# Kernel optimization log

Hardware: AMD Instinct MI355X
Metric: run time of the kernel (lower is better)

Reference implementation:

```python
import jax, jax.numpy as jnp
import numpy as np

# BatchNorm1d in eval mode with default init (gamma=1, beta=0, mean=0, var=1):
# y = x / sqrt(1 + eps)
BN_S = 1.0 / float(np.sqrt(1.0 + 1e-5))
ROI_THRESH = 0.8
DN = ('NCHW', 'OIHW', 'NCHW')


def conv(x, w, stride=1, pad=1):
    return jax.lax.conv_general_dilated(x, w, (stride, stride), ((pad, pad), (pad, pad)), dimension_numbers=DN)


def inv_conv(x, w):
    # dense equivalent of spconv.SparseInverseConv2d paired with a stride-2, pad-1, k=3 conv:
    # adjoint index map = transposed conv (lhs_dilation=2, flipped kernel, pad (1,2))
    return jax.lax.conv_general_dilated(x, jnp.flip(w, (2, 3)), (1, 1), ((1, 2), (1, 2)), lhs_dilation=(2, 2), dimension_numbers=DN)


def downsample_mask(m):
    # active-site generation rule of a stride-2, pad-1, k=3 sparse conv == 3x3/stride-2 max pool
    return jax.lax.reduce_window(m, 0.0, jax.lax.max, (1, 1, 3, 3), (1, 1, 2, 2), ((0, 0), (0, 0), (1, 1), (1, 1)))


def setup_inputs():
    key = jax.random.key(0)
    ks = jax.random.split(key, 24)
    b, n_i, H, W = 2, 4, 384, 384
    s = 0.1  # weight scale to keep activations bounded through the conv stack
    inp = {
        'x': jax.random.normal(ks[0], (b, 64, H // 4, W // 4), jnp.float32),
        'image': jax.random.normal(ks[1], (b, 3, H, W), jnp.float32),
        'masks': jax.random.uniform(ks[2], (b, n_i, H, W), jnp.float32),
        'roi_masks': jax.random.uniform(ks[3], (b, n_i, H, W), jnp.float32),
        'w1a': jax.random.normal(ks[4], (32, 4, 3, 3), jnp.float32) * s,
        'w1b': jax.random.normal(ks[5], (32, 32, 3, 3), jnp.float32) * s,
        'w2a': jax.random.normal(ks[6], (32, 32, 3, 3), jnp.float32) * s,
        'w2b': jax.random.normal(ks[7], (32, 32, 3, 3), jnp.float32) * s,
        'w4a': jax.random.normal(ks[8], (64, 32, 3, 3), jnp.float32) * s,
        'w4b': jax.random.normal(ks[9], (64, 64, 3, 3), jnp.float32) * s,
        'inv4_w': jax.random.normal(ks[10], (64, 64, 3, 3), jnp.float32) * s,
        'l4_sub_w': jax.random.normal(ks[11], (32, 64, 3, 3), jnp.float32) * s,
        'inv2_w': jax.random.normal(ks[12], (32, 32, 3, 3), jnp.float32) * s,
        'l5_sub_w': jax.random.normal(ks[13], (32, 32, 3, 3), jnp.float32) * s,
        'r4_w1': jax.random.normal(ks[14], (32, 64, 3, 3), jnp.float32) * s,
        'r4_w2': jax.random.normal(ks[15], (1, 32, 3, 3), jnp.float32) * s,
        'r4_b2': jax.random.normal(ks[16], (1,), jnp.float32) * s,
        'r1_w1': jax.random.normal(ks[17], (32, 32, 3, 3), jnp.float32) * s,
        'r1_w2': jax.random.normal(ks[18], (1, 32, 3, 3), jnp.float32) * s,
        'r1_b2': jax.random.normal(ks[19], (1,), jnp.float32) * s,
    }
    return inp


def reference(x, image, masks, roi_masks, w1a, w1b, w2a, w2b, w4a, w4b, inv4_w, l4_sub_w, inv2_w, l5_sub_w, r4_w1, r4_w2, r4_b2, r1_w1, r1_w2, r1_b2):
    # Faithful dense emulation of predict_details: SubMConv == conv(masked x)*mask,
    # stride-2 SparseConv == conv(masked x) masked by max-pooled mask,
    # SparseInverseConv == transposed conv masked by parent-resolution mask,
    # Fsp.sparse_add on shared indices == masked add, dense()-99/+99 == where(mask, v, -99).
    b, n_i, H, W = masks.shape
    N = b * n_i
    m = masks.reshape(N, 1, H, W)
    roi = roi_masks.reshape(N, 1, H, W)
    img = jnp.broadcast_to(image[:, None], (b, n_i, 3, H, W)).reshape(N, 3, H, W)
    inp = jnp.concatenate([img, m], axis=1)  # [N,4,H,W]

    mask1 = (roi > ROI_THRESH).astype(inp.dtype)
    mask2 = downsample_mask(mask1)
    mask4 = downsample_mask(mask2)

    # low_os1_module: SubMConv, ReLU, BN, SubMConv, ReLU, BN
    f = jnp.maximum(conv(inp * mask1, w1a) * mask1, 0.0) * BN_S
    fea1 = jnp.maximum(conv(f, w1b) * mask1, 0.0) * BN_S  # [N,32,H,W]
    # low_os2_module: stride-2 SparseConv, ReLU, BN, SubMConv, ReLU, BN
    g = jnp.maximum(conv(fea1, w2a, stride=2) * mask2, 0.0) * BN_S
    fea2 = jnp.maximum(conv(g, w2b) * mask2, 0.0) * BN_S  # [N,32,H/2,W/2]
    # low_os4_module
    h = jnp.maximum(conv(fea2, w4a, stride=2) * mask4, 0.0) * BN_S
    fea3 = jnp.maximum(conv(h, w4b) * mask4, 0.0) * BN_S  # [N,64,H/4,W/4]

    # gather dense OS4 features at sparse sites (batch index // n_i) + sparse_add
    xg = jnp.broadcast_to(x[:, None], (b, n_i) + x.shape[1:]).reshape(N, *x.shape[1:]) * mask4
    xs = xg + fea3

    # refine_OS4: SubMConv, BN, leaky, SubMConv(+bias); dense() with -99 off-support
    t = jax.nn.leaky_relu(conv(xs, r4_w1) * mask4 * BN_S, 0.2)
    t = (conv(t, r4_w2) + r4_b2[None, :, None, None]) * mask4
    x_os4_out = jnp.where(mask4 > 0, t, -99.0)

    # layer4: SparseInverseConv(64->64) to OS2 sites, BN, leaky, SubMConv(64->32); add fea2
    u = jax.nn.leaky_relu(inv_conv(xs, inv4_w) * mask2 * BN_S, 0.2)
    u = conv(u, l4_sub_w) * mask2 + fea2
    # layer5: SparseInverseConv(32->32) to OS1 sites, BN, leaky, SubMConv(32->32); add fea1
    v = jax.nn.leaky_relu(inv_conv(u, inv2_w) * mask1 * BN_S, 0.2)
    v = conv(v, l5_sub_w) * mask1 + fea1

    # refine_OS1
    t1 = jax.nn.leaky_relu(conv(v, r1_w1) * mask1 * BN_S, 0.2)
    t1 = (conv(t1, r1_w2) + r1_b2[None, :, None, None]) * mask1
    x_os1_out = jnp.where(mask1 > 0, t1, -99.0)
    return x_os4_out, x_os1_out
```

## Files before the change

kernel.cpp:

```cpp
#include <hip/hip_runtime.h>
#include <hip/hip_bf16.h>

using bf16 = __hip_bfloat16;
typedef unsigned char u8;
typedef short bf16x8 __attribute__((ext_vector_type(8)));
typedef short bf16x4 __attribute__((ext_vector_type(4)));
typedef float f32x4 __attribute__((ext_vector_type(4)));

#define BNS 0.9999950000374997f
#define MFMA_B16 __builtin_amdgcn_mfma_f32_16x16x32_bf16

__device__ __forceinline__ short f2bs(float v){ bf16 h = __float2bfloat16(v); return *reinterpret_cast<short*>(&h); }
__device__ __forceinline__ float s2f(short s){ union{unsigned u; float f;} x; x.u = ((unsigned)(unsigned short)s) << 16; return x.f; }
__device__ __forceinline__ float lrelu(float a){ return fmaxf(a, 0.2f*a); }
__device__ __forceinline__ bf16x8 ld8(const short* p){ return *(const bf16x8*)(p); }


__global__ __launch_bounds__(256) void k_mask1(const float* __restrict__ roi, u8* __restrict__ m1, int total){
    int i = blockIdx.x*256 + threadIdx.x;
    if (i < total) m1[i] = (roi[i] > 0.8f) ? 1 : 0;
}

__global__ __launch_bounds__(256) void k_down(const u8* __restrict__ mi, u8* __restrict__ mo,
                                              int IH, int IW, int OH, int OW){
    int p = blockIdx.x*256 + threadIdx.x;
    int n = blockIdx.y;
    if (p >= OH*OW) return;
    int oy = p / OW, ox = p - oy*OW;
    const u8* src = mi + (size_t)n*IH*IW;
    int v = 0;
    #pragma unroll
    for (int ky=0; ky<3; ky++){
        int iy = 2*oy + ky - 1;
        if ((unsigned)iy >= (unsigned)IH) continue;
        #pragma unroll
        for (int kx=0; kx<3; kx++){
            int ix = 2*ox + kx - 1;
            if ((unsigned)ix < (unsigned)IW) v |= src[iy*IW + ix];
        }
    }
    mo[(size_t)n*OH*OW + p] = (u8)v;
}

__global__ __launch_bounds__(256) void k_wprep(const float* __restrict__ w1b,
                                               const float* __restrict__ i2,
                                               const float* __restrict__ l5,
                                               const float* __restrict__ r1a,
                                               const float* __restrict__ w2b,
                                               const float* __restrict__ w2a,
                                               short* __restrict__ dst){
    int a = blockIdx.y;
    const float* src = (a==0)? w1b : (a==1)? i2 : (a==2)? l5 : (a==3)? r1a : (a==4)? w2b : w2a;
    float sc = (a==2) ? 1.0f : BNS;
    int j = blockIdx.x*256 + threadIdx.x;
    if (j < 9216){
        int co = j/288, r = j%288, ci = r/9, k = r%9;
        dst[a*9216 + k*1024 + co*32 + ci] = f2bs(src[j]*sc);
    }
}

__global__ __launch_bounds__(256) void k_wprep4(const float* __restrict__ inv4,
                                                const float* __restrict__ w4b,
                                                const float* __restrict__ l4s,
                                                const float* __restrict__ r4w1,
                                                const float* __restrict__ w4a,
                                                short* __restrict__ dst)
{
    int a = blockIdx.y;
    int j = blockIdx.x*256 + threadIdx.x;
    if (a < 2){
        if (j < 36864){
            int co = j/576, r = j%576, ci = r/9, k = r%9;
            const float* s = a ? w4b : inv4;
            dst[a*36864 + k*4096 + co*64 + ci] = f2bs(s[j]*BNS);
        }
    } else if (a < 4){
        if (j < 18432){
            int co = j/576, r = j%576, ci = r/9, k = r%9;
            const float* s = (a==2) ? l4s : r4w1;
            float sc = (a==2) ? 1.0f : BNS;
            dst[73728 + (a-2)*18432 + k*2048 + co*64 + ci] = f2bs(s[j]*sc);
        }
    } else {
        if (j < 18432){
            int co = j/288, r = j%288, ci = r/9, k = r%9;
            dst[110592 + k*2048 + co*32 + ci] = f2bs(w4a[j]*BNS);
        }
    }
}

__global__ __launch_bounds__(256) void k_wprep_misc(const float* __restrict__ w1a,
                                                    const float* __restrict__ r1w2,
                                                    const float* __restrict__ r4w2,
                                                    short* __restrict__ d1a,
                                                    short* __restrict__ dh){
    int a = blockIdx.y;
    int j = blockIdx.x*256 + threadIdx.x;
    if (a == 0){
        if (j < 2048){
            int h = j >> 10, r = j & 1023, co = r >> 5, kq = r & 31;
            int q = h*32 + kq;
            d1a[j] = (q < 36) ? f2bs(w1a[co*36 + q]*BNS) : 0;
        }
    } else {
        if (j < 4608){
            int k = j/512, r = j%512, co = r/32, ci = r%32;
            const float* s = (a==1) ? r1w2 : r4w2;
            dh[(a-1)*4608 + j] = (co == 0) ? f2bs(s[ci*9 + k]) : 0;
        }
    }
}

template<int CIN, int COUT, int EPI, int TH>
__global__ __launch_bounds__(256) void mconv_s1(const short* __restrict__ in, int H,
                                                const short* __restrict__ wT,
                                                const u8* __restrict__ mask,
                                                const float* __restrict__ res32,
                                                short* __restrict__ out, int tilesX)
{
    const int HW = H*H;
    const int HV = CIN/32, G = COUT/16, CH8 = CIN/8;
    const int SR = TH + 2;
    const int SITES = SR*18;
    const int PS = (SITES | 1)*8;
    const int U2N = TH/4;
    int tY = blockIdx.x / tilesX, tX = blockIdx.x % tilesX, n = blockIdx.z;
    int y0 = tY*TH, x0 = tX*16;

    __shared__ __align__(16) short s_in[CH8*((SITES|1)*8)];
    __shared__ u8 s_m[TH*16];

    int tid = threadIdx.x;
    const short* inN = in + (size_t)n*HW*CIN;
    for (int i = tid; i < SITES*CH8; i += 256){
        int r = i/CH8, q = i%CH8;
        int ry = r/18, rx = r%18;
        int gy = y0-1+ry, gx = x0-1+rx;
        bf16x8 v = {0,0,0,0,0,0,0,0};
        if ((unsigned)gy < (unsigned)H && (unsigned)gx < (unsigned)H)
            v = *(const bf16x8*)(inN + ((size_t)gy*H + gx)*CIN + q*8);
        *(bf16x8*)(s_in + q*PS + r*8) = v;
    }
    for (int i = tid; i < TH*16; i += 256){
        int ty = i>>4, tx = i&15;
        s_m[i] = mask[(size_t)n*HW + (y0+ty)*H + x0+tx];
    }
    __syncthreads();

    int wv = tid >> 6, lane = tid & 63;
    int nQ = lane >> 4, nn = lane & 15;

    f32x4 acc[U2N][G];
    #pragma unroll
    for (int u2=0; u2<U2N; ++u2)
        #pragma unroll
        for (int g=0; g<G; ++g) acc[u2][g] = (f32x4){0,0,0,0};

    #pragma unroll
    for (int h=0; h<HV; ++h){
        const short* bh[U2N];
        #pragma unroll
        for (int u2=0; u2<U2N; ++u2){
            int ty = u2*4 + wv;
            bh[u2] = s_in + (h*4+nQ)*PS + (ty*18 + nn)*8;
        }
        #pragma unroll
        for (int ky=0; ky<3; ++ky)
            #pragma unroll
            for (int kx=0; kx<3; ++kx){
                const int k = ky*3+kx;
                bf16x8 a[G];
                #pragma unroll
                for (int g=0; g<G; ++g)
                    a[g] = *(const bf16x8*)(wT + k*COUT*CIN + (g*16+nn)*CIN + h*32 + nQ*8);
                #pragma unroll
                for (int u2=0; u2<U2N; ++u2){
                    bf16x8 bfr = ld8(bh[u2] + (ky*18+kx)*8);
                    #pragma unroll
                    for (int g=0; g<G; ++g)
                        acc[u2][g] = MFMA_B16(a[g], bfr, acc[u2][g], 0,0,0);
                }
            }
    }

    #pragma unroll
    for (int u2=0; u2<U2N; ++u2){
        int nt = u2*4 + wv;
        int p = (y0+nt)*H + x0+nn;
        u8 m = s_m[nt*16 + nn];
        short* op = out + ((size_t)n*HW + p)*COUT;
        #pragma unroll
        for (int g=0; g<G; ++g){
            float r[4];
            #pragma unroll
            for (int e=0; e<4; ++e){
                int co = g*16 + nQ*4 + e;
                float a = acc[u2][g][e], o;
                if      (EPI == 0) o = m ? fmaxf(a,0.f) : 0.f;
                else if (EPI == 1) o = m ? lrelu(a) : 0.f;
                else o = m ? fmaxf(a,0.f) + res32[((size_t)(n>>2)*COUT + co)*(size_t)HW + p] : 0.f;
                r[e] = o;
            }
            bf16x4 w4 = {f2bs(r[0]),f2bs(r[1]),f2bs(r[2]),f2bs(r[3])};
            *(bf16x4*)(op + g*16 + nQ*4) = w4;
        }
    }
}

template<int TH>
__global__ __launch_bounds__(256) void mconv_head32(const short* __restrict__ in, int H,
                                                    const short* __restrict__ wTh,
                                                    const float* __restrict__ bias,
                                                    const u8* __restrict__ mask,
                                                    float* __restrict__ out, int tilesX)
{
    const int HW = H*H;
    const int SR = TH + 2, SITES = SR*18;
    const int PS = (SITES|1)*8;
    int tY = blockIdx.x / tilesX, tX = blockIdx.x % tilesX, n = blockIdx.z;
    int y0 = tY*TH, x0 = tX*16;

    __shared__ __align__(16) short s_in[4*((SITES|1)*8)];
    __shared__ u8 s_m[TH*16];

    int tid = threadIdx.x;
    const short* inN = in + (size_t)n*HW*32;
    for (int i = tid; i < SITES*4; i += 256){
        int r = i>>2, q = i&3;
        int ry = r/18, rx = r%18;
        int gy = y0-1+ry, gx = x0-1+rx;
        bf16x8 v = {0,0,0,0,0,0,0,0};
        if ((unsigned)gy < (unsigned)H && (unsigned)gx < (unsigned)H)
            v = *(const bf16x8*)(inN + ((size_t)gy*H + gx)*32 + q*8);
        *(bf16x8*)(s_in + q*PS + r*8) = v;
    }
    for (int i = tid; i < TH*16; i += 256){
        int ty = i>>4, tx = i&15;
        s_m[i] = mask[(size_t)n*HW + (y0+ty)*H + x0+tx];
    }
    __syncthreads();

    int wv = tid >> 6, lane = tid & 63;
    int nQ = lane >> 4, nn = lane & 15;
    float bb = bias[0];

    for (int nt = wv; nt < TH; nt += 4){
        const short* bp = s_in + nQ*PS + (nt*18 + nn)*8;
        f32x4 acc = {0,0,0,0};
        #pragma unroll
        for (int ky=0; ky<3; ++ky)
            #pragma unroll
            for (int kx=0; kx<3; ++kx){
                const int k = ky*3+kx;
                bf16x8 aw = *(const bf16x8*)(wTh + k*512 + nn*32 + nQ*8);
                bf16x8 bfr = ld8(bp + (ky*18+kx)*8);
                acc = MFMA_B16(aw, bfr, acc, 0,0,0);
            }
        if (nQ == 0){
            u8 m = s_m[nt*16 + nn];
            int p = (y0+nt)*H + x0+nn;
            out[(size_t)n*HW + p] = m ? acc[0] + bb : -99.f;
        }
    }
}

template<int COUT, int THO>
__global__ __launch_bounds__(256) void mconv_s2m(const short* __restrict__ in, int IH,
                                                 const short* __restrict__ wT,
                                                 const u8* __restrict__ mask,
                                                 short* __restrict__ out, int OH, int tilesX)
{
    const int IHW = IH*IH, OHW = OH*OH, G = COUT/16;
    const int IR = 2*THO + 1;
    const int SITES = IR*33;
    const int PS = (SITES|1)*8;
    const int ITN = THO/4;
    int tY = blockIdx.x / tilesX, tX = blockIdx.x % tilesX, n = blockIdx.z;
    int y0 = tY*THO, x0 = tX*16;

    __shared__ __align__(16) short s_in[4*((SITES|1)*8)];
    __shared__ u8 s_m[THO*16];

    int tid = threadIdx.x;
    const short* inN = in + (size_t)n*IHW*32;
    for (int i = tid; i < SITES*4; i += 256){
        int r = i>>2, q = i&3;
        int ry = r/33, rx = r%33;
        int gy = 2*y0-1+ry, gx = 2*x0-1+rx;
        bf16x8 v = {0,0,0,0,0,0,0,0};
        if ((unsigned)gy < (unsigned)IH && (unsigned)gx < (unsigned)IH)
            v = *(const bf16x8*)(inN + ((size_t)gy*IH + gx)*32 + q*8);
        *(bf16x8*)(s_in + q*PS + r*8) = v;
    }
    for (int i = tid; i < THO*16; i += 256){
        int ty = i>>4, tx = i&15;
        s_m[i] = mask[(size_t)n*OHW + (y0+ty)*OH + x0+tx];
    }
    __syncthreads();

    int wv = tid >> 6, lane = tid & 63;
    int nQ = lane >> 4, nn = lane & 15;

    f32x4 acc[ITN][G];
    #pragma unroll
    for (int it=0; it<ITN; ++it)
        #pragma unroll
        for (int g=0; g<G; ++g) acc[it][g] = (f32x4){0,0,0,0};

    const short* pb[ITN];
    #pragma unroll
    for (int it=0; it<ITN; ++it){
        int nt = it*4 + wv;
        pb[it] = s_in + nQ*PS + ((2*nt)*33 + 2*nn)*8;
    }

    #pragma unroll
    for (int ky=0; ky<3; ++ky)
        #pragma unroll
        for (int kx=0; kx<3; ++kx){
            const int k = ky*3+kx;
            bf16x8 a[G];
            #pragma unroll
            for (int g=0; g<G; ++g)
                a[g] = *(const bf16x8*)(wT + k*COUT*32 + (g*16+nn)*32 + nQ*8);
            #pragma unroll
            for (int it=0; it<ITN; ++it){
                bf16x8 bfr = ld8(pb[it] + (ky*33+kx)*8);
                #pragma unroll
                for (int g=0; g<G; ++g)
                    acc[it][g] = MFMA_B16(a[g], bfr, acc[it][g], 0,0,0);
            }
        }

    #pragma unroll
    for (int it=0; it<ITN; ++it){
        int nt = it*4 + wv;
        int p = (y0+nt)*OH + x0+nn;
        u8 m = s_m[nt*16 + nn];
        short* op = out + ((size_t)n*OHW + p)*COUT;
        #pragma unroll
        for (int g=0; g<G; ++g){
            float r[4];
            #pragma unroll
            for (int e=0; e<4; ++e) r[e] = m ? fmaxf(acc[it][g][e],0.f) : 0.f;
            bf16x4 w4 = {f2bs(r[0]),f2bs(r[1]),f2bs(r[2]),f2bs(r[3])};
            *(bf16x4*)(op + g*16 + nQ*4) = w4;
        }
    }
}

__global__ __launch_bounds__(256) void conv1ab3(const float* __restrict__ image,
                                                const float* __restrict__ masks,
                                                const u8*  __restrict__ M1,
                                                const short* __restrict__ wT1a,
                                                const short* __restrict__ wT1b,
                                                short* __restrict__ fea1)
{
    const int H = 384; const int HW = H*H;
    const int PS = 181*8;
    int tY = blockIdx.x / 48, tX = blockIdx.x % 48, n = blockIdx.z;
    int y0 = tY*16, x0 = tX*8;

    __shared__ float s_inp[4][240];
    __shared__ u8    s_m[240];
    __shared__ __align__(16) short s_ic[8*(181*8)];
    short* s_f = s_ic;

    int tid = threadIdx.x;
    for (int i = tid; i < 240; i += 256){
        int ly = i/12, lxx = i%12;
        int gy = y0-2+ly, gx = x0-2+lxx;
        bool inb = ((unsigned)gy < 384u) && ((unsigned)gx < 384u);
        u8 mv = inb ? M1[(size_t)n*HW + gy*H + gx] : 0;
        s_m[i] = mv;
        float mm = (float)mv;
        int p = gy*H + gx;
        #pragma unroll
        for (int c = 0; c < 4; ++c){
            float v = 0.f;
            if (inb) v = (c < 3) ? image[((size_t)(n>>2)*3 + c)*HW + p]
                                 : masks[(size_t)n*HW + p];
            s_inp[c][i] = v*mm;
        }
    }
    __syncthreads();

    for (int i = tid; i < 180*64; i += 256){
        int site = i >> 6, q = i & 63;
        short v = 0;
        if (q < 36){
            int ci = q/9, k = q - ci*9, ky = k/3, kx = k - ky*3;
            int fy = site/10, fx = site - fy*10;
            v = f2bs(s_inp[ci][(fy+ky)*12 + fx+kx]);
        }
        s_ic[(q>>3)*PS + site*8 + (q&7)] = v;
    }
    __syncthreads();

    int wv = tid >> 6, lane = tid & 63;
    int nQ = lane >> 4, nn = lane & 15;

    f32x4 fr[3][2];
    {
        #pragma unroll
        for (int u=0; u<3; ++u){ fr[u][0] = (f32x4){0,0,0,0}; fr[u][1] = (f32x4){0,0,0,0}; }
        #pragma unroll
        for (int h=0; h<2; ++h){
            bf16x8 fa0 = *(const bf16x8*)(wT1a + h*1024 + nn*32 + nQ*8);
            bf16x8 fa1 = *(const bf16x8*)(wT1a + h*1024 + (16+nn)*32 + nQ*8);
            #pragma unroll
            for (int u=0; u<3; ++u){
                int nt = u*4 + wv;
                int s0 = nt*16 + nn;
                int s = s0 > 179 ? 179 : s0;
                bf16x8 bfr = ld8(s_ic + (h*4+nQ)*PS + s*8);
                fr[u][0] = MFMA_B16(fa0, bfr, fr[u][0], 0,0,0);
                fr[u][1] = MFMA_B16(fa1, bfr, fr[u][1], 0,0,0);
            }
        }
    }
    __syncthreads();

    #pragma unroll
    for (int u=0; u<3; ++u){
        int nt = u*4 + wv;
        int s0 = nt*16 + nn;
        if (s0 <= 179){
            int fy = s0/10, fx = s0 - fy*10;
            u8 m = s_m[(fy+1)*12 + fx+1];
            #pragma unroll
            for (int g=0; g<2; ++g){
                float r[4];
                #pragma unroll
                for (int e=0; e<4; ++e){
                    float a = fr[u][g][e];
                    r[e] = m ? fmaxf(a,0.f) : 0.f;
                }
                bf16x4 w4 = {f2bs(r[0]),f2bs(r[1]),f2bs(r[2]),f2bs(r[3])};
                *(bf16x4*)(s_f + (g*2 + (nQ>>1))*PS + s0*8 + (nQ&1)*4) = w4;
            }
        }
    }
    __syncthreads();

    {
        f32x4 acc0[2], acc1[2];
        const short* pb[2];
        #pragma unroll
        for (int it=0; it<2; ++it){
            acc0[it] = (f32x4){0,0,0,0}; acc1[it] = (f32x4){0,0,0,0};
            int s0 = (it*4 + wv)*16 + nn;
            int ty = s0 >> 3, tx = s0 & 7;
            pb[it] = s_f + nQ*PS + (ty*10 + tx)*8;
        }
        #pragma unroll
        for (int ky=0; ky<3; ++ky)
            #pragma unroll
            for (int kx=0; kx<3; ++kx){
                const int k = ky*3+kx;
                bf16x8 a0 = *(const bf16x8*)(wT1b + k*1024 + nn*32 + nQ*8);
                bf16x8 a1 = *(const bf16x8*)(wT1b + k*1024 + (16+nn)*32 + nQ*8);
                #pragma unroll
                for (int it=0; it<2; ++it){
                    bf16x8 bfr = ld8(pb[it] + (ky*10+kx)*8);
                    acc0[it] = MFMA_B16(a0, bfr, acc0[it], 0,0,0);
                    acc1[it] = MFMA_B16(a1, bfr, acc1[it], 0,0,0);
                }
            }
        #pragma unroll
        for (int it=0; it<2; ++it){
            int s0 = (it*4 + wv)*16 + nn;
            int ty = s0 >> 3, tx = s0 & 7;
            u8 m = s_m[(ty+2)*12 + tx+2];
            short* fp = fea1 + ((size_t)n*HW + (size_t)(y0+ty)*H + (x0+tx))*32;
            #pragma unroll
            for (int g=0; g<2; ++g){
                float r[4];
                #pragma unroll
                for (int e=0; e<4; ++e){
                    float a = g ? acc1[it][e] : acc0[it][e];
                    r[e] = m ? fmaxf(a,0.f) : 0.f;
                }
                bf16x4 w4 = {f2bs(r[0]),f2bs(r[1]),f2bs(r[2]),f2bs(r[3])};
                *(bf16x4*)(fp + g*16 + nQ*4) = w4;
            }
        }
    }
}

__global__ __launch_bounds__(256) void fk_l4c(const short* __restrict__ xs,
                                              const short* __restrict__ fea2,
                                              const u8*  __restrict__ M2,
                                              const short* __restrict__ wTi4,
                                              const short* __restrict__ wTl4,
                                              short* __restrict__ u_out)
{
    const int H2 = 192, HW2 = H2*H2, H4 = 96, HW4 = H4*H4;
    const int PSX = 101*8, PSU = 325*8;
    int tY = blockIdx.x / 12, tX = blockIdx.x % 12, n = blockIdx.z;
    int y0 = tY*16, x0 = tX*16;
    int uy0 = (y0>>1) - 1, ux0 = (x0>>1) - 1;

    __shared__ __align__(16) short s_xs[8*(101*8)];
    __shared__ __align__(16) short s_ul[8*(325*8)];
    __shared__ u8 s_m[324];

    int tid = threadIdx.x;
    const short* xN = xs + (size_t)n*HW4*64;
    for (int i = tid; i < 100*8; i += 256){
        int r = i>>3, q = i&7;
        int ly = r/10, lxx = r%10;
        int gy = uy0+ly, gx = ux0+lxx;
        bf16x8 v = {0,0,0,0,0,0,0,0};
        if ((unsigned)gy < 96u && (unsigned)gx < 96u)
            v = *(const bf16x8*)(xN + ((size_t)gy*H4 + gx)*64 + q*8);
        *(bf16x8*)(s_xs + q*PSX + r*8) = v;
    }
    for (int i = tid; i < 324; i += 256){
        int ry = i/18, rx = i%18; int gy = y0-1+ry, gx = x0-1+rx;
        s_m[i] = ((unsigned)gy < 192u && (unsigned)gx < 192u) ? M2[(size_t)n*HW2 + gy*H2 + gx] : 0;
    }

    int wv = tid >> 6, lane = tid & 63;
    int nQ = lane >> 4, nn = lane & 15;

    bf16x4 pf2v[4][2];
    {
        const short* f2N = fea2 + (size_t)n*HW2*32;
        #pragma unroll
        for (int u2=0; u2<4; ++u2){
            int nt = u2*4 + wv;
            int p = (y0+nt)*H2 + x0+nn;
            const short* fp = f2N + (size_t)p*32;
            pf2v[u2][0] = *(const bf16x4*)(fp + nQ*4);
            pf2v[u2][1] = *(const bf16x4*)(fp + 16 + nQ*4);
        }
    }
    __syncthreads();

    for (int ui = wv; ui < 24; ui += 4){
        int cls = ui/6, nt = ui%6;
        int pY = cls >> 1, pX = cls & 1;
        int s0 = nt*16 + nn;
        int s = s0 > 80 ? 80 : s0;
        int jr = s/9, jc = s%9;
        int ry = 2*jr + pY, rx = 2*jc + pX;

        int tiy[4], tix[4], twk[4]; int tapN;
        if (pY == 0){
            if (pX == 0){
                tiy[0]=jr;   tix[0]=jc;   twk[0]=8;
                tiy[1]=jr;   tix[1]=jc+1; twk[1]=6;
                tiy[2]=jr+1; tix[2]=jc;   twk[2]=2;
                tiy[3]=jr+1; tix[3]=jc+1; twk[3]=0; tapN=4;
            } else {
                tiy[0]=jr;   tix[0]=jc+1; twk[0]=7;
                tiy[1]=jr+1; tix[1]=jc+1; twk[1]=1; tapN=2;
            }
        } else {
            if (pX == 0){
                tiy[0]=jr+1; tix[0]=jc;   twk[0]=5;
                tiy[1]=jr+1; tix[1]=jc+1; twk[1]=3; tapN=2;
            } else {
                tiy[0]=jr+1; tix[0]=jc+1; twk[0]=4; tapN=1;
            }
        }

        f32x4 acc[4];
        #pragma unroll
        for (int g=0; g<4; ++g) acc[g] = (f32x4){0,0,0,0};
        for (int t = 0; t < tapN; ++t){
            int off = (tiy[t]*10 + tix[t])*8;
            bf16x8 xlo = ld8(s_xs + nQ*PSX + off);
            bf16x8 xhi = ld8(s_xs + (4+nQ)*PSX + off);
            const short* wk = wTi4 + twk[t]*4096;
            #pragma unroll
            for (int g=0; g<4; ++g){
                bf16x8 alo = *(const bf16x8*)(wk + (g*16+nn)*64 + nQ*8);
                bf16x8 ahi = *(const bf16x8*)(wk + (g*16+nn)*64 + 32 + nQ*8);
                acc[g] = MFMA_B16(alo, xlo, acc[g], 0,0,0);
                acc[g] = MFMA_B16(ahi, xhi, acc[g], 0,0,0);
            }
        }
        if (s0 <= 80){
            int sidx = ry*18 + rx;
            u8 m = s_m[sidx];
            #pragma unroll
            for (int g=0; g<4; ++g){
                float r[4];
                #pragma unroll
                for (int e=0; e<4; ++e){
                    float a = acc[g][e];
                    r[e] = m ? lrelu(a) : 0.f;
                }
                bf16x4 w4 = {f2bs(r[0]),f2bs(r[1]),f2bs(r[2]),f2bs(r[3])};
                *(bf16x4*)(s_ul + ((g>>1)*4 + (g&1)*2 + (nQ>>1))*PSU + sidx*8 + (nQ&1)*4) = w4;
            }
        }
    }
    __syncthreads();

    {
        f32x4 acc0[4], acc1[4];
        const short* pv[4];
        #pragma unroll
        for (int u2=0; u2<4; ++u2){
            acc0[u2] = (f32x4){0,0,0,0}; acc1[u2] = (f32x4){0,0,0,0};
            int nt = u2*4 + wv;
            pv[u2] = s_ul + nQ*PSU + (nt*18 + nn)*8;
        }
        #pragma unroll
        for (int ky=0; ky<3; ++ky)
            #pragma unroll
            for (int kx=0; kx<3; ++kx){
                int k = ky*3+kx;
                const short* wk = wTl4 + k*2048;
                bf16x8 a0lo = *(const bf16x8*)(wk + nn*64 + nQ*8);
                bf16x8 a0hi = *(const bf16x8*)(wk + nn*64 + 32 + nQ*8);
                bf16x8 a1lo = *(const bf16x8*)(wk + (16+nn)*64 + nQ*8);
                bf16x8 a1hi = *(const bf16x8*)(wk + (16+nn)*64 + 32 + nQ*8);
                #pragma unroll
                for (int u2=0; u2<4; ++u2){
                    bf16x8 vlo = ld8(pv[u2] + (ky*18+kx)*8);
                    bf16x8 vhi = ld8(pv[u2] + 4*PSU + (ky*18+kx)*8);
                    acc0[u2] = MFMA_B16(a0lo, vlo, acc0[u2], 0,0,0);
                    acc0[u2] = MFMA_B16(a0hi, vhi, acc0[u2], 0,0,0);
                    acc1[u2] = MFMA_B16(a1lo, vlo, acc1[u2], 0,0,0);
                    acc1[u2] = MFMA_B16(a1hi, vhi, acc1[u2], 0,0,0);
                }
            }
        #pragma unroll
        for (int u2 = 0; u2 < 4; ++u2){
            int nt = u2*4 + wv;
            int p = (y0+nt)*H2 + x0+nn;
            u8 m = s_m[(nt+1)*18 + nn+1];
            short* up = u_out + ((size_t)n*HW2 + p)*32;
            #pragma unroll
            for (int g=0; g<2; ++g){
                float r[4];
                #pragma unroll
                for (int e=0; e<4; ++e){
                    float a = g ? acc1[u2][e] : acc0[u2][e];
                    r[e] = m ? a + s2f(pf2v[u2][g][e]) : 0.f;
                }
                bf16x4 w4 = {f2bs(r[0]),f2bs(r[1]),f2bs(r[2]),f2bs(r[3])};
                *(bf16x4*)(up + g*16 + nQ*4) = w4;
            }
        }
    }
}

__global__ __launch_bounds__(256) void fk_back8(const short* __restrict__ u,
                                                const short* __restrict__ fea1,
                                                const u8*  __restrict__ M1,
                                                const short* __restrict__ wTi2,
                                                const short* __restrict__ wTl5,
                                                const short* __restrict__ wTr1a,
                                                const short* __restrict__ wTr1b,
                                                const float* __restrict__ r1_b2,
                                                float* __restrict__ out1)
{
    const int H1 = 384, HW1 = H1*H1, H2 = 192, HW2 = H2*H2;
    const int PS_U = 97*8, PS_A = 309*8, PS_B = 241*8, PS_C = 181*8;
    int tY = blockIdx.x / 48, tX = blockIdx.x % 48, n = blockIdx.z;
    int y0 = tY*16, x0 = tX*8;
    int uy0 = (y0>>1) - 2, ux0 = (x0>>1) - 2;

    __shared__ __align__(16) short sP0[4*(309*8)];
    __shared__ __align__(16) short sP1[4*(241*8)];
    __shared__ u8 s_m[308];
    short* s_u  = sP1;
    short* s_vl = sP0;
    short* s_v  = sP1;
    short* s_t1 = sP0;

    int tid = threadIdx.x;
    const short* uN = u + (size_t)n*HW2*32;
    for (int i = tid; i < 96*4; i += 256){
        int r = i>>2, q = i&3;
        int ly = r >> 3, lxx = r & 7;
        int gy = uy0+ly, gx = ux0+lxx;
        bf16x8 v = {0,0,0,0,0,0,0,0};
        if ((unsigned)gy < 192u && (unsigned)gx < 192u)
            v = *(const bf16x8*)(uN + ((size_t)gy*H2 + gx)*32 + q*8);
        *(bf16x8*)(s_u + q*PS_U + r*8) = v;
    }
    for (int i = tid; i < 308; i += 256){
        int ry = i/14, rx = i%14; int gy = y0-3+ry, gx = x0-3+rx;
        s_m[i] = ((unsigned)gy < 384u && (unsigned)gx < 384u) ? M1[(size_t)n*HW1 + gy*H1 + gx] : 0;
    }

    int wv = tid >> 6, lane = tid & 63;
    int nQ = lane >> 4, nn = lane & 15;

    bf16x4 pf[4][2];
    {
        #pragma unroll
        for (int u2=0; u2<4; ++u2){
            int nt = u2*4 + wv;
            if (nt < 15){
                int s0 = nt*16 + nn;
                int vy = s0/12, vx = s0%12;
                int gY = y0-2+vy, gX = x0-2+vx;
                int gyc = gY < 0 ? 0 : (gY > 383 ? 383 : gY);
                int gxc = gX < 0 ? 0 : (gX > 383 ? 383 : gX);
                const short* f1 = fea1 + ((size_t)n*HW1 + (size_t)gyc*H1 + gxc)*32;
                pf[u2][0] = *(const bf16x4*)(f1 + nQ*4);
                pf[u2][1] = *(const bf16x4*)(f1 + 16 + nQ*4);
            }
        }
    }
    __syncthreads();

    for (int ui = wv; ui < 20; ui += 4){
        int cls = ui/5, nt = ui%5;
        int pY = cls >> 1, pX = cls & 1;
        int s0 = nt*16 + nn;
        int s = s0 > 76 ? 76 : s0;
        int jr = s/7, jc = s%7;
        int ry = 2*jr + pY, rx = 2*jc + pX;

        int tiy[4], tix[4], twk[4]; int tapN;
        if (pY == 0){
            if (pX == 0){
                tiy[0]=jr;   tix[0]=jc;   twk[0]=8;
                tiy[1]=jr;   tix[1]=jc+1; twk[1]=6;
                tiy[2]=jr+1; tix[2]=jc;   twk[2]=2;
                tiy[3]=jr+1; tix[3]=jc+1; twk[3]=0; tapN=4;
            } else {
                tiy[0]=jr;   tix[0]=jc+1; twk[0]=7;
                tiy[1]=jr+1; tix[1]=jc+1; twk[1]=1; tapN=2;
            }
        } else {
            if (pX == 0){
                tiy[0]=jr+1; tix[0]=jc;   twk[0]=5;
                tiy[1]=jr+1; tix[1]=jc+1; twk[1]=3; tapN=2;
            } else {
                tiy[0]=jr+1; tix[0]=jc+1; twk[0]=4; tapN=1;
            }
        }

        f32x4 acc0 = {0,0,0,0}, acc1 = {0,0,0,0};
        for (int t = 0; t < tapN; ++t){
            bf16x8 bfr = ld8(s_u + nQ*PS_U + (tiy[t]*8 + tix[t])*8);
            bf16x8 a0 = *(const bf16x8*)(wTi2 + twk[t]*1024 + nn*32 + nQ*8);
            bf16x8 a1 = *(const bf16x8*)(wTi2 + twk[t]*1024 + (16+nn)*32 + nQ*8);
            acc0 = MFMA_B16(a0, bfr, acc0, 0,0,0);
            acc1 = MFMA_B16(a1, bfr, acc1, 0,0,0);
        }
        if (s0 <= 76){
            int sidx = ry*14 + rx;
            u8 m = s_m[sidx];
            float r[8];
            #pragma unroll
            for (int g=0; g<2; ++g)
                #pragma unroll
                for (int e=0; e<4; ++e){
                    float a = g ? acc1[e] : acc0[e];
                    r[g*4+e] = m ? lrelu(a) : 0.f;
                }
            bf16x4 w0 = {f2bs(r[0]),f2bs(r[1]),f2bs(r[2]),f2bs(r[3])};
            bf16x4 w1 = {f2bs(r[4]),f2bs(r[5]),f2bs(r[6]),f2bs(r[7])};
            *(bf16x4*)(s_vl + (nQ>>1)*PS_A     + sidx*8 + (nQ&1)*4) = w0;
            *(bf16x4*)(s_vl + (2+(nQ>>1))*PS_A + sidx*8 + (nQ&1)*4) = w1;
        }
    }
    __syncthreads();

    {
        f32x4 acc0[4], acc1[4];
        const short* pv[4]; bool act[4];
        #pragma unroll
        for (int u2=0; u2<4; ++u2){
            acc0[u2] = (f32x4){0,0,0,0}; acc1[u2] = (f32x4){0,0,0,0};
            int nt = u2*4 + wv;
            act[u2] = (nt < 15);
            int s0 = act[u2] ? nt*16 + nn : 0;
            int vy = s0/12, vx = s0%12;
            pv[u2] = s_vl + nQ*PS_A + (vy*14 + vx)*8;
        }
        #pragma unroll
        for (int ky=0; ky<3; ++ky)
            #pragma unroll
            for (int kx=0; kx<3; ++kx){
                const int k = ky*3+kx;
                bf16x8 wb0 = *(const bf16x8*)(wTl5 + k*1024 + nn*32 + nQ*8);
                bf16x8 wb1 = *(const bf16x8*)(wTl5 + k*1024 + (16+nn)*32 + nQ*8);
                #pragma unroll
                for (int u2=0; u2<4; ++u2){
                    bf16x8 bfr = ld8(pv[u2] + (ky*14+kx)*8);
                    acc0[u2] = MFMA_B16(wb0, bfr, acc0[u2], 0,0,0);
                    acc1[u2] = MFMA_B16(wb1, bfr, acc1[u2], 0,0,0);
                }
            }
        #pragma unroll
        for (int u2 = 0; u2 < 4; ++u2){
            if (!act[u2]) continue;
            int s0 = (u2*4 + wv)*16 + nn;
            int vy = s0/12, vx = s0%12;
            u8 m = s_m[(vy+1)*14 + vx+1];
            float r[8];
            #pragma unroll
            for (int g=0; g<2; ++g)
                #pragma unroll
                for (int e=0; e<4; ++e){
                    float a = g ? acc1[u2][e] : acc0[u2][e];
                    r[g*4+e] = m ? a + s2f(pf[u2][g][e]) : 0.f;
                }
            bf16x4 w0 = {f2bs(r[0]),f2bs(r[1]),f2bs(r[2]),f2bs(r[3])};
            bf16x4 w1 = {f2bs(r[4]),f2bs(r[5]),f2bs(r[6]),f2bs(r[7])};
            *(bf16x4*)(s_v + (nQ>>1)*PS_B     + s0*8 + (nQ&1)*4) = w0;
            *(bf16x4*)(s_v + (2+(nQ>>1))*PS_B + s0*8 + (nQ&1)*4) = w1;
        }
    }
    __syncthreads();

    {
        f32x4 acc0[3], acc1[3];
        const short* pt[3];
        #pragma unroll
        for (int t=0; t<3; ++t){
            acc0[t] = (f32x4){0,0,0,0}; acc1[t] = (f32x4){0,0,0,0};
            int s0 = (wv + t*4)*16 + nn;
            int s = s0 > 179 ? 179 : s0;
            int qy = s/10, qx = s%10;
            pt[t] = s_v + nQ*PS_B + (qy*12 + qx)*8;
        }
        #pragma unroll
        for (int ky=0; ky<3; ++ky)
            #pragma unroll
            for (int kx=0; kx<3; ++kx){
                const int k = ky*3+kx;
                bf16x8 wc0 = *(const bf16x8*)(wTr1a + k*1024 + nn*32 + nQ*8);
                bf16x8 wc1 = *(const bf16x8*)(wTr1a + k*1024 + (16+nn)*32 + nQ*8);
                #pragma unroll
                for (int t=0; t<3; ++t){
                    bf16x8 bfr = ld8(pt[t] + (ky*12+kx)*8);
                    acc0[t] = MFMA_B16(wc0, bfr, acc0[t], 0,0,0);
                    acc1[t] = MFMA_B16(wc1, bfr, acc1[t], 0,0,0);
                }
            }
        #pragma unroll
        for (int t=0; t<3; ++t){
            int s0 = (wv + t*4)*16 + nn;
            if (s0 <= 179){
                int qy = s0/10, qx = s0%10;
                u8 m = s_m[(qy+2)*14 + qx+2];
                float r[8];
                #pragma unroll
                for (int g=0; g<2; ++g)
                    #pragma unroll
                    for (int e=0; e<4; ++e){
                        float a = g ? acc1[t][e] : acc0[t][e];
                        r[g*4+e] = m ? lrelu(a) : 0.f;
                    }
                bf16x4 w0 = {f2bs(r[0]),f2bs(r[1]),f2bs(r[2]),f2bs(r[3])};
                bf16x4 w1 = {f2bs(r[4]),f2bs(r[5]),f2bs(r[6]),f2bs(r[7])};
                *(bf16x4*)(s_t1 + (nQ>>1)*PS_C     + s0*8 + (nQ&1)*4) = w0;
                *(bf16x4*)(s_t1 + (2+(nQ>>1))*PS_C + s0*8 + (nQ&1)*4) = w1;
            }
        }
    }
    __syncthreads();

    {
        float bb = r1_b2[0];
        f32x4 acc[2];
        const short* pt1[2];
        #pragma unroll
        for (int u2=0; u2<2; ++u2){
            acc[u2] = (f32x4){0,0,0,0};
            int s0 = (u2*4 + wv)*16 + nn;
            int ty = s0 >> 3, tx = s0 & 7;
            pt1[u2] = s_t1 + nQ*PS_C + (ty*10 + tx)*8;
        }
        #pragma unroll
        for (int ky=0; ky<3; ++ky)
            #pragma unroll
            for (int kx=0; kx<3; ++kx){
                const int k = ky*3+kx;
                bf16x8 aw = *(const bf16x8*)(wTr1b + k*512 + nn*32 + nQ*8);
                #pragma unroll
                for (int u2=0; u2<2; ++u2){
                    bf16x8 bfr = ld8(pt1[u2] + (ky*10+kx)*8);
                    acc[u2] = MFMA_B16(aw, bfr, acc[u2], 0,0,0);
                }
            }
        if (nQ == 0){
            #pragma unroll
            for (int u2=0; u2<2; ++u2){
                int s0 = (u2*4 + wv)*16 + nn;
                int ty = s0 >> 3, tx = s0 & 7;
                u8 m = s_m[(ty+3)*14 + tx+3];
                float o = m ? acc[u2][0] + bb : -99.f;
                out1[(size_t)n*HW1 + (y0+ty)*H1 + (x0+tx)] = o;
            }
        }
    }
}


extern "C" void kernel_launch(void* const* d_in, const int* in_sizes, int n_in,
                              void* d_out, int out_size, void* d_ws, size_t ws_size,
                              hipStream_t stream)
{
    const float* x      = (const float*)d_in[0];
    const float* image  = (const float*)d_in[1];
    const float* masks  = (const float*)d_in[2];
    const float* roi    = (const float*)d_in[3];
    const float* w1a    = (const float*)d_in[4];
    const float* w1b    = (const float*)d_in[5];
    const float* w2a    = (const float*)d_in[6];
    const float* w2b    = (const float*)d_in[7];
    const float* w4a    = (const float*)d_in[8];
    const float* w4b    = (const float*)d_in[9];
    const float* inv4_w = (const float*)d_in[10];
    const float* l4_sub = (const float*)d_in[11];
    const float* inv2_w = (const float*)d_in[12];
    const float* l5_sub = (const float*)d_in[13];
    const float* r4_w1  = (const float*)d_in[14];
    const float* r4_w2  = (const float*)d_in[15];
    const float* r4_b2  = (const float*)d_in[16];
    const float* r1_w1  = (const float*)d_in[17];
    const float* r1_w2  = (const float*)d_in[18];
    const float* r1_b2  = (const float*)d_in[19];
    float* out = (float*)d_out;

    const int N = 8;
    const int H1 = 384, HW1 = 384*384;
    const int H2 = 192, HW2 = 192*192;
    const int H4 = 96,  HW4 = 96*96;

    char* wsp = (char*)d_ws;
    size_t off = 0;
    auto alloc = [&](size_t bytes) -> char* {
        char* p = wsp + off;
        off += (bytes + 255) & ~(size_t)255;
        return p;
    };
    bf16* FEA1 = (bf16*)alloc((size_t)N*32*HW1*2);
    u8*   M1   = (u8*)alloc((size_t)N*HW1);
    u8*   M2   = (u8*)alloc((size_t)N*HW2);
    u8*   M4   = (u8*)alloc((size_t)N*HW4);
    bf16* FEA2 = (bf16*)alloc((size_t)N*32*HW2*2);
    bf16* XS   = (bf16*)alloc((size_t)N*64*HW4*2);
    bf16* GU   = (bf16*)alloc((size_t)N*32*HW2*2);
    bf16* HT   = (bf16*)alloc((size_t)N*64*HW4*2);
    short* WT   = (short*)alloc(6*9216*2);
    short* WT4  = (short*)alloc((size_t)129024*2);
    short* WT1a = (short*)alloc(2048*2);
    short* WTh  = (short*)alloc(2*4608*2);
    (void)ws_size; (void)in_sizes; (void)n_in; (void)out_size;

    short* wT1b  = WT;
    short* wTi2  = WT + 9216;
    short* wTl5  = WT + 2*9216;
    short* wTr1a = WT + 3*9216;
    short* wT2b  = WT + 4*9216;
    short* wT2a  = WT + 5*9216;
    short* wTi4  = WT4;
    short* wT4b  = WT4 + 36864;
    short* wTl4  = WT4 + 73728;
    short* wTr4a = WT4 + 92160;
    short* wT4a  = WT4 + 110592;
    short* wTr1b = WTh;
    short* wTr4b = WTh + 4608;

    dim3 blk(256);

    k_mask1<<<dim3((N*HW1 + 255)/256), blk, 0, stream>>>(roi, M1, N*HW1);
    k_down<<<dim3((HW2 + 255)/256, N), blk, 0, stream>>>(M1, M2, H1, H1, H2, H2);
    k_down<<<dim3((HW4 + 255)/256, N), blk, 0, stream>>>(M2, M4, H2, H2, H4, H4);
    k_wprep<<<dim3(36, 6), blk, 0, stream>>>(w1b, inv2_w, l5_sub, r1_w1, w2b, w2a, WT);
    k_wprep4<<<dim3(144, 5), blk, 0, stream>>>(inv4_w, w4b, l4_sub, r4_w1, w4a, WT4);
    k_wprep_misc<<<dim3(18, 3), blk, 0, stream>>>(w1a, r1_w2, r4_w2, WT1a, WTh);

    conv1ab3<<<dim3(1152, 1, N), blk, 0, stream>>>(image, masks, M1, WT1a, wT1b, (short*)FEA1);
    mconv_s2m<32,8><<<dim3(288, 1, N), blk, 0, stream>>>((const short*)FEA1, H1, wT2a, M2, (short*)GU, H2, 12);
    mconv_s1<32,32,0,8><<<dim3(288, 1, N), blk, 0, stream>>>((const short*)GU, H2, wT2b, M2, nullptr, (short*)FEA2, 12);
    mconv_s2m<64,4><<<dim3(144, 1, N), blk, 0, stream>>>((const short*)FEA2, H2, wT4a, M4, (short*)HT, H4, 6);
    mconv_s1<64,64,3,4><<<dim3(144, 1, N), blk, 0, stream>>>((const short*)HT, H4, wT4b, M4, x, (short*)XS, 6);

    mconv_s1<64,32,1,4><<<dim3(144, 1, N), blk, 0, stream>>>((const short*)XS, H4, wTr4a, M4, nullptr, (short*)HT, 6);
    mconv_head32<4><<<dim3(144, 1, N), blk, 0, stream>>>((const short*)HT, H4, wTr4b, r4_b2, M4, out, 6);

    fk_l4c<<<dim3(144, 1, N), blk, 0, stream>>>((const short*)XS, (const short*)FEA2, M2,
                                                wTi4, wTl4, (short*)GU);

    fk_back8<<<dim3(1152, 1, N), blk, 0, stream>>>((const short*)GU, (const short*)FEA1, M1,
                                                   wTi2, wTl5, wTr1a, wTr1b, r1_b2,
                                                   out + (size_t)N*HW4);
}
```

Before: 606.3 us.

## Compact active sites per stage in fused OS1 kernel to skip masked MFMA work

The fused OS1 kernel now builds per-stage lists of active (mask=1) sites in shared memory with atomic counters, and runs each MFMA conv stage only over compacted 16-site groups of active positions instead of every position in the tile. Inactive output pixels are written as -99 up front, and the staging buffers are zero-filled before each stage so inactive neighbours read as zero. With about 20% active sites this is meant to cut matrix work substantially. In exchange it adds list-building passes, atomics, extra zero-fill loops and barriers, a per-wave imbalance in the inverse-conv stage (one parity class per wave), and fea1 loads that are now issued inside the loop rather than prefetched.

Result: faster. 551.3 us (-9.1%).

```diff
diff --git a/kernel.cpp b/kernel.cpp
--- a/kernel.cpp
+++ b/kernel.cpp
@@ -669,18 +669,26 @@
     __shared__ __align__(16) short sP0[4*(309*8)];
     __shared__ __align__(16) short sP1[4*(241*8)];
     __shared__ u8 s_m[308];
+    __shared__ int s_cnt[7];
+    __shared__ unsigned s_lA[4*80];
+    __shared__ unsigned s_lB[240];
+    __shared__ unsigned s_lC[180];
+    __shared__ unsigned s_lD[128];
     short* s_u  = sP1;
     short* s_vl = sP0;
     short* s_v  = sP1;
     short* s_t1 = sP0;
 
     int tid = threadIdx.x;
+    const bf16x8 Z8 = {0,0,0,0,0,0,0,0};
+
+    if (tid < 7) s_cnt[tid] = 0;
     const short* uN = u + (size_t)n*HW2*32;
     for (int i = tid; i < 96*4; i += 256){
         int r = i>>2, q = i&3;
         int ly = r >> 3, lxx = r & 7;
         int gy = uy0+ly, gx = ux0+lxx;
-        bf16x8 v = {0,0,0,0,0,0,0,0};
+        bf16x8 v = Z8;
         if ((unsigned)gy < 192u && (unsigned)gx < 192u)
             v = *(const bf16x8*)(uN + ((size_t)gy*H2 + gx)*32 + q*8);
         *(bf16x8*)(s_u + q*PS_U + r*8) = v;
@@ -689,175 +697,165 @@
         int ry = i/14, rx = i%14; int gy = y0-3+ry, gx = x0-3+rx;
         s_m[i] = ((unsigned)gy < 384u && (unsigned)gx < 384u) ? M1[(size_t)n*HW1 + gy*H1 + gx] : 0;
     }
+    for (int i = tid; i < 4*309; i += 256)
+        *(bf16x8*)(s_vl + i*8) = Z8;
+    __syncthreads();
+
+    for (int i = tid; i < 308; i += 256){
+        if (s_m[i]){
+            int ry = i/14, rx = i - ry*14;
+            int cls = ((ry&1)<<1) | (rx&1);
+            int jr = ry>>1, jc = rx>>1;
+            int idx = atomicAdd(&s_cnt[cls], 1);
+            s_lA[cls*80 + idx] = ((unsigned)i<<16) | (unsigned)(jr*8+jc);
+        }
+    }
+    for (int i = tid; i < 240; i += 256){
+        int vy = i/12, vx = i - vy*12;
+        if (s_m[(vy+1)*14 + vx+1]){
+            int idx = atomicAdd(&s_cnt[4], 1);
+            s_lB[idx] = ((unsigned)i<<16) | (unsigned)(vy*14+vx);
+        }
+    }
+    for (int i = tid; i < 180; i += 256){
+        int qy = i/10, qx = i - qy*10;
+        if (s_m[(qy+2)*14 + qx+2]){
+            int idx = atomicAdd(&s_cnt[5], 1);
+            s_lC[idx] = ((unsigned)i<<16) | (unsigned)(qy*12+qx);
+        }
+    }
+    for (int i = tid; i < 128; i += 256){
+        int ty = i>>3, tx = i&7;
+        if (s_m[(ty+3)*14 + tx+3]){
+            int idx = atomicAdd(&s_cnt[6], 1);
+            s_lD[idx] = ((unsigned)i<<16) | (unsigned)(ty*10+tx);
+        } else {
+            out1[(size_t)n*HW1 + (size_t)(y0+ty)*H1 + (x0+tx)] = -99.f;
+        }
+    }
+    __syncthreads();
 
     int wv = tid >> 6, lane = tid & 63;
     int nQ = lane >> 4, nn = lane & 15;
 
-    bf16x4 pf[4][2];
     {
-        #pragma unroll
-        for (int u2=0; u2<4; ++u2){
-            int nt = u2*4 + wv;
-            if (nt < 15){
-                int s0 = nt*16 + nn;
-                int vy = s0/12, vx = s0%12;
-                int gY = y0-2+vy, gX = x0-2+vx;
-                int gyc = gY < 0 ? 0 : (gY > 383 ? 383 : gY);
-                int gxc = gX < 0 ? 0 : (gX > 383 ? 383 : gX);
-                const short* f1 = fea1 + ((size_t)n*HW1 + (size_t)gyc*H1 + gxc)*32;
-                pf[u2][0] = *(const bf16x4*)(f1 + nQ*4);
-                pf[u2][1] = *(const bf16x4*)(f1 + 16 + nQ*4);
-            }
-        }
-    }
-    __syncthreads();
-
-    for (int ui = wv; ui < 20; ui += 4){
-        int cls = ui/5, nt = ui%5;
-        int pY = cls >> 1, pX = cls & 1;
-        int s0 = nt*16 + nn;
-        int s = s0 > 76 ? 76 : s0;
-        int jr = s/7, jc = s%7;
-        int ry = 2*jr + pY, rx = 2*jc + pX;
-
-        int tiy[4], tix[4], twk[4]; int tapN;
-        if (pY == 0){
-            if (pX == 0){
-                tiy[0]=jr;   tix[0]=jc;   twk[0]=8;
-                tiy[1]=jr;   tix[1]=jc+1; twk[1]=6;
-                tiy[2]=jr+1; tix[2]=jc;   twk[2]=2;
-                tiy[3]=jr+1; tix[3]=jc+1; twk[3]=0; tapN=4;
-            } else {
-                tiy[0]=jr;   tix[0]=jc+1; twk[0]=7;
-                tiy[1]=jr+1; tix[1]=jc+1; twk[1]=1; tapN=2;
-            }
-        } else {
-            if (pX == 0){
-                tiy[0]=jr+1; tix[0]=jc;   twk[0]=5;
-                tiy[1]=jr+1; tix[1]=jc+1; twk[1]=3; tapN=2;
-            } else {
-                tiy[0]=jr+1; tix[0]=jc+1; twk[0]=4; tapN=1;
-            }
-        }
-
-        f32x4 acc0 = {0,0,0,0}, acc1 = {0,0,0,0};
-        for (int t = 0; t < tapN; ++t){
-            bf16x8 bfr = ld8(s_u + nQ*PS_U + (tiy[t]*8 + tix[t])*8);
-            bf16x8 a0 = *(const bf16x8*)(wTi2 + twk[t]*1024 + nn*32 + nQ*8);
-            bf16x8 a1 = *(const bf16x8*)(wTi2 + twk[t]*1024 + (16+nn)*32 + nQ*8);
-            acc0 = MFMA_B16(a0, bfr, acc0, 0,0,0);
-            acc1 = MFMA_B16(a1, bfr, acc1, 0,0,0);
-        }
-        if (s0 <= 76){
-            int sidx = ry*14 + rx;
-            u8 m = s_m[sidx];
-            float r[8];
-            #pragma unroll
-            for (int g=0; g<2; ++g)
-                #pragma unroll
-                for (int e=0; e<4; ++e){
-                    float a = g ? acc1[e] : acc0[e];
-                    r[g*4+e] = m ? lrelu(a) : 0.f;
-                }
-            bf16x4 w0 = {f2bs(r[0]),f2bs(r[1]),f2bs(r[2]),f2bs(r[3])};
-            bf16x4 w1 = {f2bs(r[4]),f2bs(r[5]),f2bs(r[6]),f2bs(r[7])};
-            *(bf16x4*)(s_vl + (nQ>>1)*PS_A     + sidx*8 + (nQ&1)*4) = w0;
-            *(bf16x4*)(s_vl + (2+(nQ>>1))*PS_A + sidx*8 + (nQ&1)*4) = w1;
-        }
-    }
-    __syncthreads();
-
-    {
-        f32x4 acc0[4], acc1[4];
-        const short* pv[4]; bool act[4];
-        #pragma unroll
-        for (int u2=0; u2<4; ++u2){
-            acc0[u2] = (f32x4){0,0,0,0}; acc1[u2] = (f32x4){0,0,0,0};
-            int nt = u2*4 + wv;
-            act[u2] = (nt < 15);
-            int s0 = act[u2] ? nt*16 + nn : 0;
-            int vy = s0/12, vx = s0%12;
-            pv[u2] = s_vl + nQ*PS_A + (vy*14 + vx)*8;
-        }
-        #pragma unroll
-        for (int ky=0; ky<3; ++ky)
-            #pragma unroll
-            for (int kx=0; kx<3; ++kx){
-                const int k = ky*3+kx;
-                bf16x8 wb0 = *(const bf16x8*)(wTl5 + k*1024 + nn*32 + nQ*8);
-                bf16x8 wb1 = *(const bf16x8*)(wTl5 + k*1024 + (16+nn)*32 + nQ*8);
-                #pragma unroll
-                for (int u2=0; u2<4; ++u2){
-                    bf16x8 bfr = ld8(pv[u2] + (ky*14+kx)*8);
-                    acc0[u2] = MFMA_B16(wb0, bfr, acc0[u2], 0,0,0);
-                    acc1[u2] = MFMA_B16(wb1, bfr, acc1[u2], 0,0,0);
-                }
-            }
-        #pragma unroll
-        for (int u2 = 0; u2 < 4; ++u2){
-            if (!act[u2]) continue;
-            int s0 = (u2*4 + wv)*16 + nn;
-            int vy = s0/12, vx = s0%12;
-            u8 m = s_m[(vy+1)*14 + vx+1];
-            float r[8];
-            #pragma unroll
-            for (int g=0; g<2; ++g)
-                #pragma unroll
-                for (int e=0; e<4; ++e){
-                    float a = g ? acc1[u2][e] : acc0[u2][e];
-                    r[g*4+e] = m ? a + s2f(pf[u2][g][e]) : 0.f;
-                }
-            bf16x4 w0 = {f2bs(r[0]),f2bs(r[1]),f2bs(r[2]),f2bs(r[3])};
-            bf16x4 w1 = {f2bs(r[4]),f2bs(r[5]),f2bs(r[6]),f2bs(r[7])};
-            *(bf16x4*)(s_v + (nQ>>1)*PS_B     + s0*8 + (nQ&1)*4) = w0;
-            *(bf16x4*)(s_v + (2+(nQ>>1))*PS_B + s0*8 + (nQ&1)*4) = w1;
-        }
-    }
-    __syncthreads();
-
-    {
-        f32x4 acc0[3], acc1[3];
-        const short* pt[3];
-        #pragma unroll
-        for (int t=0; t<3; ++t){
-            acc0[t] = (f32x4){0,0,0,0}; acc1[t] = (f32x4){0,0,0,0};
-            int s0 = (wv + t*4)*16 + nn;
-            int s = s0 > 179 ? 179 : s0;
-            int qy = s/10, qx = s%10;
-            pt[t] = s_v + nQ*PS_B + (qy*12 + qx)*8;
-        }
-        #pragma unroll
-        for (int ky=0; ky<3; ++ky)
-            #pragma unroll
-            for (int kx=0; kx<3; ++kx){
-                const int k = ky*3+kx;
-                bf16x8 wc0 = *(const bf16x8*)(wTr1a + k*1024 + nn*32 + nQ*8);
-                bf16x8 wc1 = *(const bf16x8*)(wTr1a + k*1024 + (16+nn)*32 + nQ*8);
-                #pragma unroll
-                for (int t=0; t<3; ++t){
-                    bf16x8 bfr = ld8(pt[t] + (ky*12+kx)*8);
-                    acc0[t] = MFMA_B16(wc0, bfr, acc0[t], 0,0,0);
-                    acc1[t] = MFMA_B16(wc1, bfr, acc1[t], 0,0,0);
-                }
-            }
-        #pragma unroll
-        for (int t=0; t<3; ++t){
-            int s0 = (wv + t*4)*16 + nn;
-            if (s0 <= 179){
-                int qy = s0/10, qx = s0%10;
-                u8 m = s_m[(qy+2)*14 + qx+2];
+        const int tN_[4]   = {4,2,2,1};
+        const int tOff[4][4] = {{0,1,8,9},{1,9,9,9},{8,9,9,9},{9,9,9,9}};
+        const int tWk [4][4] = {{8,6,2,0},{7,1,1,1},{5,3,3,3},{4,4,4,4}};
+        int cnt = s_cnt[wv];
+        int tn = tN_[wv];
+        for (int base = 0; base < cnt; base += 16){
+            int slot = base + nn;
+            bool on = slot < cnt;
+            unsigned e = s_lA[wv*80 + (on ? slot : 0)];
+            int rb = e & 0xffff;
+            f32x4 acc0 = {0,0,0,0}, acc1 = {0,0,0,0};
+            for (int t = 0; t < tn; ++t){
+                bf16x8 bfr = ld8(s_u + nQ*PS_U + (rb + tOff[wv][t])*8);
+                const short* wp = wTi2 + tWk[wv][t]*1024;
+                bf16x8 a0 = *(const bf16x8*)(wp + nn*32 + nQ*8);
+                bf16x8 a1 = *(const bf16x8*)(wp + (16+nn)*32 + nQ*8);
+                acc0 = MFMA_B16(a0, bfr, acc0, 0,0,0);
+                acc1 = MFMA_B16(a1, bfr, acc1, 0,0,0);
+            }
+            if (on){
+                int sidx = e >> 16;
                 float r[8];
                 #pragma unroll
                 for (int g=0; g<2; ++g)
                     #pragma unroll
-                    for (int e=0; e<4; ++e){
-                        float a = g ? acc1[t][e] : acc0[t][e];
-                        r[g*4+e] = m ? lrelu(a) : 0.f;
-                    }
+                    for (int ee=0; ee<4; ++ee)
+                        r[g*4+ee] = lrelu(g ? acc1[ee] : acc0[ee]);
                 bf16x4 w0 = {f2bs(r[0]),f2bs(r[1]),f2bs(r[2]),f2bs(r[3])};
                 bf16x4 w1 = {f2bs(r[4]),f2bs(r[5]),f2bs(r[6]),f2bs(r[7])};
-                *(bf16x4*)(s_t1 + (nQ>>1)*PS_C     + s0*8 + (nQ&1)*4) = w0;
-                *(bf16x4*)(s_t1 + (2+(nQ>>1))*PS_C + s0*8 + (nQ&1)*4) = w1;
+                *(bf16x4*)(s_vl + (nQ>>1)*PS_A     + sidx*8 + (nQ&1)*4) = w0;
+                *(bf16x4*)(s_vl + (2+(nQ>>1))*PS_A + sidx*8 + (nQ&1)*4) = w1;
+            }
+        }
+    }
+    __syncthreads();
+
+    for (int i = tid; i < 4*241; i += 256)
+        *(bf16x8*)(s_v + i*8) = Z8;
+    __syncthreads();
+
+    {
+        int cnt = s_cnt[4];
+        for (int base = wv*16; base < cnt; base += 64){
+            int slot = base + nn;
+            bool on = slot < cnt;
+            unsigned e = s_lB[on ? slot : 0];
+            int rb = e & 0xffff;
+            int wr = e >> 16;
+            int vy = wr/12, vx = wr - vy*12;
+            const short* f1 = fea1 + ((size_t)n*HW1 + (size_t)(y0-2+vy)*H1 + (x0-2+vx))*32;
+            bf16x4 p0 = *(const bf16x4*)(f1 + nQ*4);
+            bf16x4 p1 = *(const bf16x4*)(f1 + 16 + nQ*4);
+            const short* pv = s_vl + nQ*PS_A + rb*8;
+            f32x4 acc0 = {0,0,0,0}, acc1 = {0,0,0,0};
+            #pragma unroll
+            for (int ky=0; ky<3; ++ky)
+                #pragma unroll
+                for (int kx=0; kx<3; ++kx){
+                    const int k = ky*3+kx;
+                    bf16x8 wb0 = *(const bf16x8*)(wTl5 + k*1024 + nn*32 + nQ*8);
+                    bf16x8 wb1 = *(const bf16x8*)(wTl5 + k*1024 + (16+nn)*32 + nQ*8);
+                    bf16x8 bfr = ld8(pv + (ky*14+kx)*8);
+                    acc0 = MFMA_B16(wb0, bfr, acc0, 0,0,0);
+                    acc1 = MFMA_B16(wb1, bfr, acc1, 0,0,0);
+                }
+            if (on){
+                float r[8];
+                #pragma unroll
+                for (int ee=0; ee<4; ++ee){
+                    r[ee]   = acc0[ee] + s2f(p0[ee]);
+                    r[4+ee] = acc1[ee] + s2f(p1[ee]);
+                }
+                bf16x4 w0 = {f2bs(r[0]),f2bs(r[1]),f2bs(r[2]),f2bs(r[3])};
+                bf16x4 w1 = {f2bs(r[4]),f2bs(r[5]),f2bs(r[6]),f2bs(r[7])};
+                *(bf16x4*)(s_v + (nQ>>1)*PS_B     + wr*8 + (nQ&1)*4) = w0;
+                *(bf16x4*)(s_v + (2+(nQ>>1))*PS_B + wr*8 + (nQ&1)*4) = w1;
+            }
+        }
+    }
+    __syncthreads();
+
+    for (int i = tid; i < 4*181; i += 256)
+        *(bf16x8*)(s_t1 + i*8) = Z8;
+    __syncthreads();
+
+    {
+        int cnt = s_cnt[5];
+        for (int base = wv*16; base < cnt; base += 64){
+            int slot = base + nn;
+            bool on = slot < cnt;
+            unsigned e = s_lC[on ? slot : 0];
+            int rb = e & 0xffff;
+            const short* pv = s_v + nQ*PS_B + rb*8;
+            f32x4 acc0 = {0,0,0,0}, acc1 = {0,0,0,0};
+            #pragma unroll
+            for (int ky=0; ky<3; ++ky)
+                #pragma unroll
+                for (int kx=0; kx<3; ++kx){
+                    const int k = ky*3+kx;
+                    bf16x8 wc0 = *(const bf16x8*)(wTr1a + k*1024 + nn*32 + nQ*8);
+                    bf16x8 wc1 = *(const bf16x8*)(wTr1a + k*1024 + (16+nn)*32 + nQ*8);
+                    bf16x8 bfr = ld8(pv + (ky*12+kx)*8);
+                    acc0 = MFMA_B16(wc0, bfr, acc0, 0,0,0);
+                    acc1 = MFMA_B16(wc1, bfr, acc1, 0,0,0);
+                }
+            if (on){
+                int wr = e >> 16;
+                float r[8];
+                #pragma unroll
+                for (int g=0; g<2; ++g)
+                    #pragma unroll
+                    for (int ee=0; ee<4; ++ee)
+                        r[g*4+ee] = lrelu(g ? acc1[ee] : acc0[ee]);
+                bf16x4 w0 = {f2bs(r[0]),f2bs(r[1]),f2bs(r[2]),f2bs(r[3])};
+                bf16x4 w1 = {f2bs(r[4]),f2bs(r[5]),f2bs(r[6]),f2bs(r[7])};
+                *(bf16x4*)(s_t1 + (nQ>>1)*PS_C     + wr*8 + (nQ&1)*4) = w0;
+                *(bf16x4*)(s_t1 + (2+(nQ>>1))*PS_C + wr*8 + (nQ&1)*4) = w1;
             }
         }
     }
@@ -865,35 +863,27 @@
 
     {
         float bb = r1_b2[0];
-        f32x4 acc[2];
-        const short* pt1[2];
-        #pragma unroll
-        for (int u2=0; u2<2; ++u2){
-            acc[u2] = (f32x4){0,0,0,0};
-            int s0 = (u2*4 + wv)*16 + nn;
-            int ty = s0 >> 3, tx = s0 & 7;
-            pt1[u2] = s_t1 + nQ*PS_C + (ty*10 + tx)*8;
-        }
-        #pragma unroll
-        for (int ky=0; ky<3; ++ky)
-            #pragma unroll
-            for (int kx=0; kx<3; ++kx){
-                const int k = ky*3+kx;
-                bf16x8 aw = *(const bf16x8*)(wTr1b + k*512 + nn*32 + nQ*8);
-                #pragma unroll
-                for (int u2=0; u2<2; ++u2){
-                    bf16x8 bfr = ld8(pt1[u2] + (ky*10+kx)*8);
-                    acc[u2] = MFMA_B16(aw, bfr, acc[u2], 0,0,0);
-                }
-            }
-        if (nQ == 0){
-            #pragma unroll
-            for (int u2=0; u2<2; ++u2){
-                int s0 = (u2*4 + wv)*16 + nn;
-                int ty = s0 >> 3, tx = s0 & 7;
-                u8 m = s_m[(ty+3)*14 + tx+3];
-                float o = m ? acc[u2][0] + bb : -99.f;
-                out1[(size_t)n*HW1 + (y0+ty)*H1 + (x0+tx)] = o;
+        int cnt = s_cnt[6];
+        for (int base = wv*16; base < cnt; base += 64){
+            int slot = base + nn;
+            bool on = slot < cnt;
+            unsigned e = s_lD[on ? slot : 0];
+            int rb = e & 0xffff;
+            const short* pt = s_t1 + nQ*PS_C + rb*8;
+            f32x4 acc = {0,0,0,0};
+            #pragma unroll
+            for (int ky=0; ky<3; ++ky)
+                #pragma unroll
+                for (int kx=0; kx<3; ++kx){
+                    const int k = ky*3+kx;
+                    bf16x8 aw = *(const bf16x8*)(wTr1b + k*512 + nn*32 + nQ*8);
+                    bf16x8 bfr = ld8(pt + (ky*10+kx)*8);
+                    acc = MFMA_B16(aw, bfr, acc, 0,0,0);
+                }
+            if (on && nQ == 0){
+                int wr = e >> 16;
+                int ty = wr >> 3, tx = wr & 7;
+                out1[(size_t)n*HW1 + (size_t)(y0+ty)*H1 + (x0+tx)] = acc[0] + bb;
             }
         }
     }
```
